# Kernel tuning notes

Measured on AMD Instinct MI355X. Metric: run time of the kernel, lower is better.

Reference implementation:

```python
import jax, jax.numpy as jnp
import numpy as np

# ---- static config (mirrors init_kwargs) ----
N, E, G = 10000, 120000, 32
F_NODE, F_EDGE = 64, 16
H, HEADS, L, R = 128, 4, 3, 4
ID_DIM, REL_DIM = 32, 8
NUM_IDS, NUM_CLASSES = 5000, 10
FFN_H, HEAD_H = 256, 128
GRID_SIZE, SPLINE_ORDER = 5, 3
NC = GRID_SIZE + SPLINE_ORDER  # n spline coeffs per input = 8
GRID = jnp.asarray(np.arange(-SPLINE_ORDER, GRID_SIZE + SPLINE_ORDER + 1, dtype=np.float32) * (2.0 / GRID_SIZE) - 1.0)  # [12], grid_range=(-1,1)
NEG = -1e30


def _b_splines(x, grid):
    # x: [B, in] -> bases [B, in, NC]  (Cox-de Boor, as in efficient-kan)
    x = x[..., None]
    bases = ((x >= grid[:-1]) & (x < grid[1:])).astype(x.dtype)
    for p in range(1, SPLINE_ORDER + 1):
        left = (x - grid[:-(p + 1)]) / (grid[p:-1] - grid[:-(p + 1)]) * bases[..., :-1]
        right = (grid[p + 1:] - x) / (grid[p + 1:] - grid[1:-p]) * bases[..., 1:]
        bases = left + right
    return bases


def _kan_linear(x, base_w, spline_w, scaler, grid):
    # base path: SiLU(x) @ W_base^T ; spline path: b_splines(x) contracted with scaled spline weights
    base = jax.nn.silu(x) @ base_w.T
    spline = jnp.einsum('big,oig->bo', _b_splines(x, grid), spline_w * scaler[..., None])
    return base + spline


def _ln(x, g, b, eps=1e-5):
    mu = x.mean(-1, keepdims=True)
    var = ((x - mu) ** 2).mean(-1, keepdims=True)
    return (x - mu) * jax.lax.rsqrt(var + eps) * g + b


def _forward(x, edge_attr, id_emb, in_W, in_b, Wl, bl, Wr, br, We, att, gat_bias,
             rel_gate, rel_emb, ln1_g, ln1_b, ln2_g, ln2_b,
             ffn1_base, ffn1_spline, ffn1_scaler, ffn2_base, ffn2_spline, ffn2_scaler,
             ro_g, ro_b, head1_base, head1_spline, head1_scaler, head2_base, head2_spline, head2_scaler,
             id_token, edge_index, edge_type, batch):
    grid = GRID
    # input proj: concat(id embedding) -> Linear -> SiLU (dropout = identity, eval)
    h = jnp.concatenate([x, id_emb[id_token]], axis=-1)
    h = jax.nn.silu(h @ in_W + in_b)
    src, tgt = edge_index[0], edge_index[1]
    for l in range(L):
        gates = jax.nn.softmax(rel_gate[l])  # all relations present
        h_msg = jnp.zeros_like(h)
        for r in range(R):
            # GATv2Conv (heads=4, concat=False, add_self_loops=False)
            xl = (h @ Wl[l, r] + bl[l, r]).reshape(N, HEADS, H)
            xr = (h @ Wr[l, r] + br[l, r]).reshape(N, HEADS, H)
            # edge feature = concat(edge_attr, rel_emb[r]) @ We, split to avoid materializing the concat
            e = (edge_attr @ We[l, r, :F_EDGE] + rel_emb[l, r] @ We[l, r, F_EDGE:]).reshape(E, HEADS, H)
            z = jax.nn.leaky_relu(xl[src] + xr[tgt] + e, 0.2)   # [E, heads, H]
            score = jnp.einsum('ehd,hd->eh', z, att[l, r])
            mask = (edge_type == r)[:, None]
            score = jnp.where(mask, score, NEG)
            m = jax.ops.segment_max(score, tgt, num_segments=N)  # per-target softmax max
            ex = jnp.where(mask, jnp.exp(score - m[tgt]), 0.0)
            denom = jax.ops.segment_sum(ex, tgt, num_segments=N)
            alpha = ex / jnp.maximum(denom[tgt], 1e-16)          # [E, heads]
            agg = jax.ops.segment_sum(xl[src] * alpha[..., None], tgt, num_segments=N)
            h_r = agg.mean(axis=1) + gat_bias[l, r]              # concat=False -> head mean + bias
            h_msg = h_msg + gates[r] * h_r
        h = _ln(h + h_msg, ln1_g[l], ln1_b[l])
        # KAN FFN: KANLinear(H->FFN_H) -> KANLinear(FFN_H->H)
        h_ffn = _kan_linear(h, ffn1_base[l], ffn1_spline[l], ffn1_scaler[l], grid)
        h_ffn = _kan_linear(h_ffn, ffn2_base[l], ffn2_spline[l], ffn2_scaler[l], grid)
        h = _ln(h + h_ffn, ln2_g[l], ln2_b[l])
    # readout: mean+max pool per graph
    cnt = jax.ops.segment_sum(jnp.ones((N,), h.dtype), batch, num_segments=G)
    h_mean = jax.ops.segment_sum(h, batch, num_segments=G) / jnp.maximum(cnt, 1.0)[:, None]
    h_max = jax.ops.segment_max(h, batch, num_segments=G)
    h_max = jnp.where(jnp.isfinite(h_max), h_max, 0.0)
    g = _ln(jnp.concatenate([h_mean, h_max], axis=-1), ro_g, ro_b)
    # KAN head: KANLinear(2H->HEAD_H) -> KANLinear(HEAD_H->NUM_CLASSES)
    g = _kan_linear(g, head1_base, head1_spline, head1_scaler, grid)
    logits = _kan_linear(g, head2_base, head2_spline, head2_scaler, grid)
    return logits


def setup_inputs():
    key = jax.random.key(0)
    ks = iter(jax.random.split(key, 48))
    n = lambda shape, s=0.05: jax.random.normal(next(ks), shape, dtype=jnp.float32) * s
    d = {}
    d['x'] = jax.random.normal(next(ks), (N, F_NODE), dtype=jnp.float32)
    d['edge_attr'] = jax.random.normal(next(ks), (E, F_EDGE), dtype=jnp.float32)
    d['id_token'] = jax.random.randint(next(ks), (N,), 0, NUM_IDS + 1)
    d['edge_index'] = jax.random.randint(next(ks), (2, E), 0, N)
    d['edge_type'] = jax.random.randint(next(ks), (E,), 0, R)
    d['batch'] = jnp.sort(jax.random.randint(next(ks), (N,), 0, G))
    d['id_emb'] = n((NUM_IDS + 1, ID_DIM), 0.1)
    d['in_W'] = n((F_NODE + ID_DIM, H))
    d['in_b'] = jnp.zeros((H,), jnp.float32)
    d['Wl'] = n((L, R, H, HEADS * H)); d['bl'] = jnp.zeros((L, R, HEADS * H), jnp.float32)
    d['Wr'] = n((L, R, H, HEADS * H)); d['br'] = jnp.zeros((L, R, HEADS * H), jnp.float32)
    d['We'] = n((L, R, F_EDGE + REL_DIM, HEADS * H))
    d['att'] = n((L, R, HEADS, H), 0.1)
    d['gat_bias'] = jnp.zeros((L, R, H), jnp.float32)
    d['rel_gate'] = n((L, R), 0.1)
    d['rel_emb'] = n((L, R, REL_DIM), 0.1)
    d['ln1_g'] = jnp.ones((L, H), jnp.float32); d['ln1_b'] = jnp.zeros((L, H), jnp.float32)
    d['ln2_g'] = jnp.ones((L, H), jnp.float32); d['ln2_b'] = jnp.zeros((L, H), jnp.float32)
    d['ffn1_base'] = n((L, FFN_H, H)); d['ffn1_spline'] = n((L, FFN_H, H, NC)); d['ffn1_scaler'] = jnp.ones((L, FFN_H, H), jnp.float32)
    d['ffn2_base'] = n((L, H, FFN_H)); d['ffn2_spline'] = n((L, H, FFN_H, NC)); d['ffn2_scaler'] = jnp.ones((L, H, FFN_H), jnp.float32)
    d['ro_g'] = jnp.ones((2 * H,), jnp.float32); d['ro_b'] = jnp.zeros((2 * H,), jnp.float32)
    d['head1_base'] = n((HEAD_H, 2 * H)); d['head1_spline'] = n((HEAD_H, 2 * H, NC)); d['head1_scaler'] = jnp.ones((HEAD_H, 2 * H), jnp.float32)
    d['head2_base'] = n((NUM_CLASSES, HEAD_H)); d['head2_spline'] = n((NUM_CLASSES, HEAD_H, NC)); d['head2_scaler'] = jnp.ones((NUM_CLASSES, HEAD_H), jnp.float32)
    return d


def reference(x, edge_attr, id_emb, in_W, in_b, Wl, bl, Wr, br, We, att, gat_bias,
              rel_gate, rel_emb, ln1_g, ln1_b, ln2_g, ln2_b,
              ffn1_base, ffn1_spline, ffn1_scaler, ffn2_base, ffn2_spline, ffn2_scaler,
              ro_g, ro_b, head1_base, head1_spline, head1_scaler, head2_base, head2_spline, head2_scaler,
              id_token, edge_index, edge_type, batch):
    return _forward(x, edge_attr, id_emb, in_W, in_b, Wl, bl, Wr, br, We, att, gat_bias,
                    rel_gate, rel_emb, ln1_g, ln1_b, ln2_g, ln2_b,
                    ffn1_base, ffn1_spline, ffn1_scaler, ffn2_base, ffn2_spline, ffn2_scaler,
                    ro_g, ro_b, head1_base, head1_spline, head1_scaler, head2_base, head2_spline, head2_scaler,
                    id_token, edge_index, edge_type, batch)
```

## Files before the change

### kernel.cpp

```cpp
#include <hip/hip_runtime.h>
#include <cstdint>
#include <cstddef>

#define NN      10000
#define NE      120000
#define NG      32
#define FNODE   64
#define FEDGE   16
#define HID     128
#define NHEADS  4
#define NL      3
#define NR      4
#define IDDIM   32
#define RELDIM  8
#define FFNH    256
#define HEADH   128
#define NCLS    10

#define NCHUNK  128
#define SCTOT   (NN * NR)
#define SCBLK   ((SCTOT + 255) / 256)

typedef __attribute__((ext_vector_type(8))) short short8;
typedef __attribute__((ext_vector_type(4))) float floatx4;

__device__ __forceinline__ float silu_f(float x) { return x / (1.f + expf(-x)); }
__device__ __forceinline__ ushort f2bf(float f) {
  unsigned u = __float_as_uint(f);
  return (ushort)((u + 0x7FFFu + ((u >> 16) & 1u)) >> 16);
}
__device__ __forceinline__ float bf2f(ushort h) { return __uint_as_float((unsigned)h << 16); }

__device__ __forceinline__ void kan_bases(float x, float* out8) {
  float bb[11];
#pragma unroll
  for (int j = 0; j < 11; ++j) {
    float t0 = (j - 3) * 0.4f - 1.f;
    float t1 = (j - 2) * 0.4f - 1.f;
    bb[j] = (x >= t0 && x < t1) ? 1.f : 0.f;
  }
  {
    const float inv = 1.f / 0.4f;
#pragma unroll
    for (int j = 0; j < 10; ++j) {
      float tj = (j - 3) * 0.4f - 1.f, tjp1 = (j - 1) * 0.4f - 1.f;
      bb[j] = ((x - tj) * bb[j] + (tjp1 - x) * bb[j + 1]) * inv;
    }
  }
  {
    const float inv = 1.f / 0.8f;
#pragma unroll
    for (int j = 0; j < 9; ++j) {
      float tj = (j - 3) * 0.4f - 1.f, tjp1 = (j) * 0.4f - 1.f;
      bb[j] = ((x - tj) * bb[j] + (tjp1 - x) * bb[j + 1]) * inv;
    }
  }
  {
    const float inv = 1.f / 1.2000001f;
#pragma unroll
    for (int j = 0; j < 8; ++j) {
      float tj = (j - 3) * 0.4f - 1.f, tjp1 = (j + 1) * 0.4f - 1.f;
      bb[j] = ((x - tj) * bb[j] + (tjp1 - x) * bb[j + 1]) * inv;
    }
  }
#pragma unroll
  for (int j = 0; j < 8; ++j) out8[j] = bb[j];
}

__global__ __launch_bounds__(256) void gemm_bf3(
    const ushort* __restrict__ Ahg, const ushort* __restrict__ Alg,
    const ushort* __restrict__ Bhg, const ushort* __restrict__ Blg,
    const float* __restrict__ bias, float* __restrict__ C,
    int M, int K, int N) {
  constexpr int LDA = 68;
  __shared__ __align__(16) ushort Ah[128 * LDA];
  __shared__ __align__(16) ushort Al[128 * LDA];
  __shared__ __align__(16) ushort Bh[64 * LDA];
  __shared__ __align__(16) ushort Bl[64 * LDA];
  const int tid = threadIdx.x;
  const int lane = tid & 63, wave = tid >> 6;
  const int lrow = lane & 15, quad = lane >> 4;
  const int bm = blockIdx.y * 128, bn = blockIdx.x * 64;
  floatx4 acc[2][4] = {};
  for (int k0 = 0; k0 < K; k0 += 64) {
#pragma unroll
    for (int i = 0; i < 4; ++i) {
      int c = tid + i * 256;
      int row = c >> 3, col8 = c & 7;
      int gr = bm + row;
      uint4 vh = make_uint4(0, 0, 0, 0), vl = make_uint4(0, 0, 0, 0);
      if (gr < M) {
        vh = *(const uint4*)(Ahg + (size_t)gr * K + k0 + col8 * 8);
        vl = *(const uint4*)(Alg + (size_t)gr * K + k0 + col8 * 8);
      }
      *(uint4*)&Ah[row * LDA + col8 * 8] = vh;
      *(uint4*)&Al[row * LDA + col8 * 8] = vl;
    }
#pragma unroll
    for (int i = 0; i < 2; ++i) {
      int c = tid + i * 256;
      int row = c >> 3, col8 = c & 7;
      *(uint4*)&Bh[row * LDA + col8 * 8] = *(const uint4*)(Bhg + (size_t)(bn + row) * K + k0 + col8 * 8);
      *(uint4*)&Bl[row * LDA + col8 * 8] = *(const uint4*)(Blg + (size_t)(bn + row) * K + k0 + col8 * 8);
    }
    __syncthreads();
#pragma unroll
    for (int kk = 0; kk < 64; kk += 32) {
      int kof = kk + quad * 8;
      const int ra0 = (wave * 32 + lrow) * LDA + kof;
      const int ra1 = (wave * 32 + 16 + lrow) * LDA + kof;
      short8 ah0 = *(const short8*)&Ah[ra0];
      short8 ah1 = *(const short8*)&Ah[ra1];
      short8 al0 = *(const short8*)&Al[ra0];
      short8 al1 = *(const short8*)&Al[ra1];
      short8 bh[4], blo[4];
#pragma unroll
      for (int nt = 0; nt < 4; ++nt) {
        int rb = (nt * 16 + lrow) * LDA + kof;
        bh[nt]  = *(const short8*)&Bh[rb];
        blo[nt] = *(const short8*)&Bl[rb];
      }
#pragma unroll
      for (int nt = 0; nt < 4; ++nt) {
        acc[0][nt] = __builtin_amdgcn_mfma_f32_16x16x32_bf16(ah0, bh[nt],  acc[0][nt], 0, 0, 0);
        acc[1][nt] = __builtin_amdgcn_mfma_f32_16x16x32_bf16(ah1, bh[nt],  acc[1][nt], 0, 0, 0);
        acc[0][nt] = __builtin_amdgcn_mfma_f32_16x16x32_bf16(al0, bh[nt],  acc[0][nt], 0, 0, 0);
        acc[1][nt] = __builtin_amdgcn_mfma_f32_16x16x32_bf16(al1, bh[nt],  acc[1][nt], 0, 0, 0);
        acc[0][nt] = __builtin_amdgcn_mfma_f32_16x16x32_bf16(ah0, blo[nt], acc[0][nt], 0, 0, 0);
        acc[1][nt] = __builtin_amdgcn_mfma_f32_16x16x32_bf16(ah1, blo[nt], acc[1][nt], 0, 0, 0);
      }
    }
    __syncthreads();
  }
#pragma unroll
  for (int mt = 0; mt < 2; ++mt) {
#pragma unroll
    for (int nt = 0; nt < 4; ++nt) {
#pragma unroll
      for (int reg = 0; reg < 4; ++reg) {
        int row = bm + wave * 32 + mt * 16 + quad * 4 + reg;
        int col = bn + nt * 16 + lrow;
        if (row < M) {
          float v = acc[mt][nt][reg];
          if (bias) v += bias[col];
          C[(size_t)row * N + col] = v;
        }
      }
    }
  }
}

template<int BM, int SPLIT>
__global__ __launch_bounds__(256) void gemm_kan(
    const float* __restrict__ A, const ushort* __restrict__ Bhg, const ushort* __restrict__ Blg,
    float* __restrict__ C, int M, int In, int N) {
  const int K = In * 9;
  const int ntiles = K >> 6;
  const int per = (ntiles + SPLIT - 1) / SPLIT;
  const int kt0 = blockIdx.z * per;
  const int kt1 = (kt0 + per < ntiles) ? (kt0 + per) : ntiles;
  constexpr int LDA = 68;
  __shared__ __align__(16) ushort Ah[BM * LDA];
  __shared__ __align__(16) ushort Al[BM * LDA];
  __shared__ __align__(16) ushort Bh[64 * LDA];
  __shared__ __align__(16) ushort Bl[64 * LDA];
  const int tid = threadIdx.x;
  const int lane = tid & 63, wave = tid >> 6;
  const int lrow = lane & 15, quad = lane >> 4;
  const int bm = blockIdx.y * BM, bn = blockIdx.x * 64;
  constexpr int MT = BM / 64;
  floatx4 acc[MT][4] = {};
  for (int kt = kt0; kt < kt1; ++kt) {
    int k0 = kt << 6;
    if (k0 < In) {
#pragma unroll
      for (int i = 0; i < BM / 16; ++i) {
        int c = tid + i * 256;
        int row = c >> 4, col4 = c & 15;
        int gr = bm + row;
        float4 v = make_float4(0.f, 0.f, 0.f, 0.f);
        if (gr < M) v = *(const float4*)(A + (size_t)gr * In + k0 + col4 * 4);
        float vv[4] = {silu_f(v.x), silu_f(v.y), silu_f(v.z), silu_f(v.w)};
        ushort h0 = f2bf(vv[0]), h1 = f2bf(vv[1]), h2 = f2bf(vv[2]), h3 = f2bf(vv[3]);
        ushort l0 = f2bf(vv[0] - bf2f(h0)), l1 = f2bf(vv[1] - bf2f(h1));
        ushort l2 = f2bf(vv[2] - bf2f(h2)), l3 = f2bf(vv[3] - bf2f(h3));
        *(uint2*)&Ah[row * LDA + col4 * 4] =
          make_uint2((unsigned)h0 | ((unsigned)h1 << 16), (unsigned)h2 | ((unsigned)h3 << 16));
        *(uint2*)&Al[row * LDA + col4 * 4] =
          make_uint2((unsigned)l0 | ((unsigned)l1 << 16), (unsigned)l2 | ((unsigned)l3 << 16));
      }
    } else {
      int i0 = (k0 - In) >> 3;
      if (tid < BM * 2) {
        int row = tid >> 1, half = tid & 1;
        int gr = bm + row;
        float4 v = make_float4(0.f, 0.f, 0.f, 0.f);
        if (gr < M) v = *(const float4*)(A + (size_t)gr * In + i0 + half * 4);
        float vv[4] = {v.x, v.y, v.z, v.w};
#pragma unroll
        for (int jj = 0; jj < 4; ++jj) {
          float b8[8];
          kan_bases(vv[jj], b8);
          unsigned hu[4], lu[4];
#pragma unroll
          for (int q = 0; q < 4; ++q) {
            ushort ha = f2bf(b8[2 * q]), hb = f2bf(b8[2 * q + 1]);
            ushort la = f2bf(b8[2 * q] - bf2f(ha)), lb = f2bf(b8[2 * q + 1] - bf2f(hb));
            hu[q] = (unsigned)ha | ((unsigned)hb << 16);
            lu[q] = (unsigned)la | ((unsigned)lb << 16);
          }
          int cbase = (half * 4 + jj) * 8;
          *(uint4*)&Ah[row * LDA + cbase] = make_uint4(hu[0], hu[1], hu[2], hu[3]);
          *(uint4*)&Al[row * LDA + cbase] = make_uint4(lu[0], lu[1], lu[2], lu[3]);
        }
      }
    }
#pragma unroll
    for (int i = 0; i < 2; ++i) {
      int c = tid + i * 256;
      int row = c >> 3, col8 = c & 7;
      *(uint4*)&Bh[row * LDA + col8 * 8] = *(const uint4*)(Bhg + (size_t)(bn + row) * K + k0 + col8 * 8);
      *(uint4*)&Bl[row * LDA + col8 * 8] = *(const uint4*)(Blg + (size_t)(bn + row) * K + k0 + col8 * 8);
    }
    __syncthreads();
#pragma unroll
    for (int kk = 0; kk < 64; kk += 32) {
      int kof = kk + quad * 8;
      short8 ah[MT], al[MT];
#pragma unroll
      for (int mt = 0; mt < MT; ++mt) {
        int ra = (wave * (BM / 4) + mt * 16 + lrow) * LDA + kof;
        ah[mt] = *(const short8*)&Ah[ra];
        al[mt] = *(const short8*)&Al[ra];
      }
      short8 bh[4], blo[4];
#pragma unroll
      for (int nt = 0; nt < 4; ++nt) {
        int rb = (nt * 16 + lrow) * LDA + kof;
        bh[nt]  = *(const short8*)&Bh[rb];
        blo[nt] = *(const short8*)&Bl[rb];
      }
#pragma unroll
      for (int nt = 0; nt < 4; ++nt) {
#pragma unroll
        for (int mt = 0; mt < MT; ++mt) {
          acc[mt][nt] = __builtin_amdgcn_mfma_f32_16x16x32_bf16(ah[mt], bh[nt],  acc[mt][nt], 0, 0, 0);
          acc[mt][nt] = __builtin_amdgcn_mfma_f32_16x16x32_bf16(al[mt], bh[nt],  acc[mt][nt], 0, 0, 0);
          acc[mt][nt] = __builtin_amdgcn_mfma_f32_16x16x32_bf16(ah[mt], blo[nt], acc[mt][nt], 0, 0, 0);
        }
      }
    }
    __syncthreads();
  }
#pragma unroll
  for (int mt = 0; mt < MT; ++mt) {
#pragma unroll
    for (int nt = 0; nt < 4; ++nt) {
#pragma unroll
      for (int reg = 0; reg < 4; ++reg) {
        int row = bm + wave * (BM / 4) + mt * 16 + quad * 4 + reg;
        int col = bn + nt * 16 + lrow;
        if (row < M) atomicAdd(&C[(size_t)row * N + col], acc[mt][nt][reg]);
      }
    }
  }
}

__global__ void conv_wT2(const float* __restrict__ Wl, const float* __restrict__ Wr,
                         const float* __restrict__ bl, const float* __restrict__ br,
                         ushort* __restrict__ WTh, ushort* __restrict__ WTl,
                         float* __restrict__ bout, int total) {
  int i = blockIdx.x * 256 + threadIdx.x;
  if (i >= total) return;
  int g2 = i / (2048 * 128), rem = i % (2048 * 128);
  int n = rem >> 7, k = rem & 127;
  int l = g2 >> 1, pair = g2 & 1;
  int r = pair * 2 + (n >> 10);
  int nsub = n & 1023;
  int nn = nsub & 511;
  int g = l * NR + r;
  const float* W = (nsub < 512) ? Wl : Wr;
  float v = W[(size_t)g * 65536 + (size_t)k * 512 + nn];
  ushort hi = f2bf(v);
  WTh[i] = hi;
  WTl[i] = f2bf(v - bf2f(hi));
  if (k == 0) bout[g2 * 2048 + n] = ((nsub < 512) ? bl : br)[g * 512 + nn];
}

__global__ void build_kan_wT(const float* __restrict__ base_w, const float* __restrict__ spline_w,
                             const float* __restrict__ scaler,
                             ushort* __restrict__ BTh, ushort* __restrict__ BTl,
                             int In, int Out) {
  int i = blockIdx.x * 256 + threadIdx.x;
  if (i >= In * 9 * Out) return;
  int o = i / (In * 9), k = i % (In * 9);
  float v;
  if (k < In) v = base_w[(size_t)o * In + k];
  else {
    int q = k - In, ii = q >> 3, gq = q & 7;
    v = spline_w[((size_t)o * In + ii) * 8 + gq] * scaler[(size_t)o * In + ii];
  }
  ushort hi = f2bf(v);
  BTh[i] = hi;
  BTl[i] = f2bf(v - bf2f(hi));
}

__global__ __launch_bounds__(128) void input_proj(
    const float* __restrict__ x, const float* __restrict__ id_emb,
    const int* __restrict__ id_token, const float* __restrict__ inW,
    const float* __restrict__ inb, float* __restrict__ h,
    ushort* __restrict__ hh, ushort* __restrict__ hl) {
  int n = blockIdx.x, j = threadIdx.x;
  __shared__ float s[FNODE + IDDIM];
  if (j < FNODE) s[j] = x[(size_t)n * FNODE + j];
  else if (j < FNODE + IDDIM) s[j] = id_emb[(size_t)id_token[n] * IDDIM + (j - FNODE)];
  __syncthreads();
  float acc = inb[j];
#pragma unroll
  for (int k = 0; k < FNODE + IDDIM; ++k) acc = fmaf(s[k], inW[k * HID + j], acc);
  float v = silu_f(acc);
  h[(size_t)n * HID + j] = v;
  ushort hi = f2bf(v);
  hh[(size_t)n * HID + j] = hi;
  hl[(size_t)n * HID + j] = f2bf(v - bf2f(hi));
}

__global__ __launch_bounds__(512) void layer_prep(
    const float* __restrict__ rel_gate, const float* __restrict__ gat_bias,
    const float* __restrict__ rel_emb, const float* __restrict__ We, int l,
    float* __restrict__ gates, float* __restrict__ msg_bias, float* __restrict__ erel) {
  int j = threadIdx.x;
  float g[NR]; float mx = -1e30f;
  for (int r = 0; r < NR; ++r) { g[r] = rel_gate[l * NR + r]; mx = fmaxf(mx, g[r]); }
  float s = 0.f;
  for (int r = 0; r < NR; ++r) { g[r] = expf(g[r] - mx); s += g[r]; }
  for (int r = 0; r < NR; ++r) g[r] /= s;
  if (j < NR) gates[j] = g[j];
  if (j < HID) {
    float b = 0.f;
    for (int r = 0; r < NR; ++r) b = fmaf(g[r], gat_bias[((size_t)(l * NR + r)) * HID + j], b);
    msg_bias[j] = b;
  }
  for (int r = 0; r < NR; ++r) {
    const float* Wer = We + ((size_t)(l * NR + r)) * 24 * 512;
    const float* re  = rel_emb + (l * NR + r) * RELDIM;
    float acc = 0.f;
#pragma unroll
    for (int q = 0; q < RELDIM; ++q) acc = fmaf(re[q], Wer[(FEDGE + q) * 512 + j], acc);
    erel[r * 512 + j] = acc;
  }
}

__global__ void fill_zero(float* __restrict__ p, int n) {
  int i = blockIdx.x * 256 + threadIdx.x;
  if (i < n) p[i] = 0.f;
}
__global__ void fill_zero_i(int* __restrict__ p, int n) {
  int i = blockIdx.x * 256 + threadIdx.x;
  if (i < n) p[i] = 0;
}

__global__ void csr_count2(const int* __restrict__ eidx, const int* __restrict__ etype,
                           int* __restrict__ deg2) {
  int e = blockIdx.x * 256 + threadIdx.x;
  if (e < NE) atomicAdd(&deg2[eidx[NE + e] * NR + etype[e]], 1);
}

__global__ __launch_bounds__(256) void scan_p1(const int* __restrict__ deg2,
                                               int* __restrict__ tmp_incl, int* __restrict__ bsum) {
  __shared__ int ps[256];
  int t = threadIdx.x, blk = blockIdx.x;
  int i = blk * 256 + t;
  int v = (i < SCTOT) ? deg2[i] : 0;
  ps[t] = v;
  __syncthreads();
  for (int o = 1; o < 256; o <<= 1) {
    int u = (t >= o) ? ps[t - o] : 0;
    __syncthreads();
    ps[t] += u;
    __syncthreads();
  }
  if (i < SCTOT) tmp_incl[i] = ps[t];
  if (t == 255) bsum[blk] = ps[255];
}
__global__ __launch_bounds__(256) void scan_p2(const int* __restrict__ bsum, int* __restrict__ boff) {
  __shared__ int ps[256];
  int t = threadIdx.x;
  int v = (t < SCBLK) ? bsum[t] : 0;
  ps[t] = v;
  __syncthreads();
  for (int o = 1; o < 256; o <<= 1) {
    int u = (t >= o) ? ps[t - o] : 0;
    __syncthreads();
    ps[t] += u;
    __syncthreads();
  }
  if (t < SCBLK) boff[t] = ps[t] - v;
}
__global__ __launch_bounds__(256) void scan_p3(const int* __restrict__ deg2,
                                               const int* __restrict__ tmp_incl,
                                               const int* __restrict__ boff,
                                               int* __restrict__ in_off2, int* __restrict__ cursor2) {
  int t = threadIdx.x, blk = blockIdx.x;
  int i = blk * 256 + t;
  if (i < SCTOT) {
    int excl = boff[blk] + tmp_incl[i] - deg2[i];
    in_off2[i] = excl;
    cursor2[i] = excl;
  }
  if (i == 0) in_off2[SCTOT] = NE;
}

__global__ void csr_scatter2(const int* __restrict__ eidx, const int* __restrict__ etype,
                             int* __restrict__ cursor2,
                             int* __restrict__ in_e2, int* __restrict__ in_s2) {
  int e = blockIdx.x * 256 + threadIdx.x;
  if (e < NE) {
    int pos = atomicAdd(&cursor2[eidx[NE + e] * NR + etype[e]], 1);
    in_e2[pos] = e;
    in_s2[pos] = eidx[e];
  }
}

__global__ __launch_bounds__(256) void gat_node6(
    const int* __restrict__ in_off2, const int* __restrict__ in_e2, const int* __restrict__ in_s2,
    const float* __restrict__ eattr, const float* __restrict__ xlr,
    const float* __restrict__ We_base, const float* __restrict__ erel_base,
    const float* __restrict__ att_base, const float* __restrict__ gates,
    int rbase, float* __restrict__ hmsg) {
  __shared__ __align__(16) float WeL[16 * 512];
  __shared__ __align__(16) float sAgg[4][512];
  int tid = threadIdx.x;
  int rs = blockIdx.y;
  int r = rbase + rs;
  const float* We_r = We_base + (size_t)rs * 24 * 512;
  for (int i = tid; i < 16 * 512 / 4; i += 256)
    *(float4*)&WeL[i * 4] = *(const float4*)&We_r[i * 4];
  __syncthreads();
  float gr = gates[r] * 0.25f;
  int lane = tid & 63, wave = tid >> 6;
  int n = blockIdx.x * 4 + wave;
  if (n >= NN) return;
  int roff = rs * 1024;
  const int cA = lane * 4;
  const int cB = 256 + lane * 4;
  const float* xrb = xlr + (size_t)n * 2048 + roff + 512;
  float4 xrA = *(const float4*)(xrb + cA);
  float4 xrB = *(const float4*)(xrb + cB);
  float4 attA = *(const float4*)(att_base + rs * 512 + cA);
  float4 attB = *(const float4*)(att_base + rs * 512 + cB);
  float4 erA  = *(const float4*)(erel_base + rs * 512 + cA);
  float4 erB  = *(const float4*)(erel_base + rs * 512 + cB);
  float mA = -1e30f, mB = -1e30f, lsA = 0.f, lsB = 0.f;
  float4 accA = make_float4(0.f, 0.f, 0.f, 0.f);
  float4 accB = make_float4(0.f, 0.f, 0.f, 0.f);
  int e0 = in_off2[n * NR + r];
  int cnt = in_off2[n * NR + r + 1] - e0;
  float4 pxA, pxB, pe0, pe1, pe2, pe3;
  int eN = 0, sN = 0;
  if (cnt > 0) {
    int eC = in_e2[e0], sC = in_s2[e0];
    if (cnt > 1) { eN = in_e2[e0 + 1]; sN = in_s2[e0 + 1]; }
    const float* xls = xlr + (size_t)sC * 2048 + roff;
    pxA = *(const float4*)(xls + cA);
    pxB = *(const float4*)(xls + cB);
    const float4* eap = (const float4*)(eattr + (size_t)eC * 16);
    pe0 = eap[0]; pe1 = eap[1]; pe2 = eap[2]; pe3 = eap[3];
  }
  for (int j = 0; j < cnt; ++j) {
    float4 xA = pxA, xB = pxB;
    float ea[16] = {pe0.x, pe0.y, pe0.z, pe0.w, pe1.x, pe1.y, pe1.z, pe1.w,
                    pe2.x, pe2.y, pe2.z, pe2.w, pe3.x, pe3.y, pe3.z, pe3.w};
    if (j + 1 < cnt) {
      int eC = eN, sC = sN;
      if (j + 2 < cnt) { eN = in_e2[e0 + j + 2]; sN = in_s2[e0 + j + 2]; }
      const float* xls = xlr + (size_t)sC * 2048 + roff;
      pxA = *(const float4*)(xls + cA);
      pxB = *(const float4*)(xls + cB);
      const float4* eap = (const float4*)(eattr + (size_t)eC * 16);
      pe0 = eap[0]; pe1 = eap[1]; pe2 = eap[2]; pe3 = eap[3];
    }
    float4 etA = erA, etB = erB;
#pragma unroll
    for (int k = 0; k < 16; ++k) {
      float4 wA = *(const float4*)&WeL[k * 512 + cA];
      float4 wB = *(const float4*)&WeL[k * 512 + cB];
      etA.x = fmaf(ea[k], wA.x, etA.x); etA.y = fmaf(ea[k], wA.y, etA.y);
      etA.z = fmaf(ea[k], wA.z, etA.z); etA.w = fmaf(ea[k], wA.w, etA.w);
      etB.x = fmaf(ea[k], wB.x, etB.x); etB.y = fmaf(ea[k], wB.y, etB.y);
      etB.z = fmaf(ea[k], wB.z, etB.z); etB.w = fmaf(ea[k], wB.w, etB.w);
    }
    float sA, sB;
    {
      float z0 = xA.x + xrA.x + etA.x; z0 = (z0 > 0.f) ? z0 : 0.2f * z0;
      float z1 = xA.y + xrA.y + etA.y; z1 = (z1 > 0.f) ? z1 : 0.2f * z1;
      float z2 = xA.z + xrA.z + etA.z; z2 = (z2 > 0.f) ? z2 : 0.2f * z2;
      float z3 = xA.w + xrA.w + etA.w; z3 = (z3 > 0.f) ? z3 : 0.2f * z3;
      sA = z0 * attA.x + z1 * attA.y + z2 * attA.z + z3 * attA.w;
      z0 = xB.x + xrB.x + etB.x; z0 = (z0 > 0.f) ? z0 : 0.2f * z0;
      z1 = xB.y + xrB.y + etB.y; z1 = (z1 > 0.f) ? z1 : 0.2f * z1;
      z2 = xB.z + xrB.z + etB.z; z2 = (z2 > 0.f) ? z2 : 0.2f * z2;
      z3 = xB.w + xrB.w + etB.w; z3 = (z3 > 0.f) ? z3 : 0.2f * z3;
      sB = z0 * attB.x + z1 * attB.y + z2 * attB.z + z3 * attB.w;
    }
#pragma unroll
    for (int o = 1; o <= 16; o <<= 1) {
      sA += __shfl_xor(sA, o, 64);
      sB += __shfl_xor(sB, o, 64);
    }
    {
      float mn = fmaxf(mA, sA);
      float sc = expf(mA - mn), we = expf(sA - mn);
      mA = mn; lsA = lsA * sc + we;
      accA.x = accA.x * sc + we * xA.x; accA.y = accA.y * sc + we * xA.y;
      accA.z = accA.z * sc + we * xA.z; accA.w = accA.w * sc + we * xA.w;
    }
    {
      float mn = fmaxf(mB, sB);
      float sc = expf(mB - mn), we = expf(sB - mn);
      mB = mn; lsB = lsB * sc + we;
      accB.x = accB.x * sc + we * xB.x; accB.y = accB.y * sc + we * xB.y;
      accB.z = accB.z * sc + we * xB.z; accB.w = accB.w * sc + we * xB.w;
    }
  }
  float invA = 1.f / fmaxf(lsA, 1e-16f);
  float invB = 1.f / fmaxf(lsB, 1e-16f);
  *(float4*)&sAgg[wave][cA] = make_float4(accA.x * invA, accA.y * invA, accA.z * invA, accA.w * invA);
  *(float4*)&sAgg[wave][cB] = make_float4(accB.x * invB, accB.y * invB, accB.z * invB, accB.w * invB);
  float o0 = sAgg[wave][lane]       + sAgg[wave][128 + lane]
           + sAgg[wave][256 + lane] + sAgg[wave][384 + lane];
  float o1 = sAgg[wave][64 + lane]  + sAgg[wave][192 + lane]
           + sAgg[wave][320 + lane] + sAgg[wave][448 + lane];
  size_t base = (size_t)n * HID;
  atomicAdd(&hmsg[base + lane],      gr * o0);
  atomicAdd(&hmsg[base + 64 + lane], gr * o1);
}

__global__ __launch_bounds__(64) void ln128(
    float* __restrict__ h, const float* __restrict__ add, const float* __restrict__ bvec,
    const float* __restrict__ g, const float* __restrict__ b,
    ushort* __restrict__ hh, ushort* __restrict__ hl) {
  int n = blockIdx.x, lane = threadIdx.x;
  size_t base = (size_t)n * HID;
  float x0 = h[base + lane] + add[base + lane];
  float x1 = h[base + 64 + lane] + add[base + 64 + lane];
  if (bvec) { x0 += bvec[lane]; x1 += bvec[64 + lane]; }
  float s = x0 + x1;
#pragma unroll
  for (int m = 32; m > 0; m >>= 1) s += __shfl_xor(s, m, 64);
  float mu = s * (1.f / 128.f);
  float d0 = x0 - mu, d1 = x1 - mu;
  float q = d0 * d0 + d1 * d1;
#pragma unroll
  for (int m = 32; m > 0; m >>= 1) q += __shfl_xor(q, m, 64);
  float inv = 1.f / sqrtf(q * (1.f / 128.f) + 1e-5f);
  float o0 = d0 * inv * g[lane] + b[lane];
  float o1 = d1 * inv * g[64 + lane] + b[64 + lane];
  h[base + lane]      = o0;
  h[base + 64 + lane] = o1;
  if (hh) {
    ushort i0 = f2bf(o0), i1 = f2bf(o1);
    hh[base + lane] = i0;        hh[base + 64 + lane] = i1;
    hl[base + lane] = f2bf(o0 - bf2f(i0));
    hl[base + 64 + lane] = f2bf(o1 - bf2f(i1));
  }
}

__global__ void expand_f32(const float* __restrict__ v, float* __restrict__ u, int In, int rows) {
  int i = blockIdx.x * 256 + threadIdx.x;
  if (i >= rows * In) return;
  int n = i / In, c = i % In;
  float x = v[(size_t)n * In + c];
  size_t base = (size_t)n * In * 9;
  u[base + c] = silu_f(x);
  float b8[8];
  kan_bases(x, b8);
  float* ub = u + base + In + (size_t)c * 8;
#pragma unroll
  for (int gq = 0; gq < 8; ++gq) ub[gq] = b8[gq];
}

__global__ __launch_bounds__(128) void pool_part(
    const float* __restrict__ h, const int* __restrict__ batch,
    float* __restrict__ psum, float* __restrict__ pmax, float* __restrict__ pcnt) {
  __shared__ float sS[NG][HID];
  __shared__ float sM[NG][HID];
  __shared__ int sC[NG];
  int d = threadIdx.x, blk = blockIdx.x;
  const float NEGINF = __uint_as_float(0xff800000u);
  for (int i = d; i < NG * HID; i += 128) {
    ((float*)sS)[i] = 0.f;
    ((float*)sM)[i] = NEGINF;
  }
  if (d < NG) sC[d] = 0;
  __syncthreads();
  const int CH = (NN + NCHUNK - 1) / NCHUNK;
  int n0 = blk * CH, n1 = (n0 + CH < NN) ? n0 + CH : NN;
  for (int n = n0; n < n1; ++n) {
    int g = batch[n];
    float v = h[(size_t)n * HID + d];
    sS[g][d] += v;
    sM[g][d] = fmaxf(sM[g][d], v);
    if (d == 0) sC[g]++;
  }
  __syncthreads();
  for (int i = d; i < NG * HID; i += 128) {
    psum[(size_t)blk * NG * HID + i] = ((float*)sS)[i];
    pmax[(size_t)blk * NG * HID + i] = ((float*)sM)[i];
  }
  if (d < NG) pcnt[blk * NG + d] = (float)sC[d];
}

__global__ __launch_bounds__(256) void pool_final2(
    const float* __restrict__ psum, const float* __restrict__ pmax,
    const float* __restrict__ pcnt, const float* __restrict__ rog,
    const float* __restrict__ rob, float* __restrict__ gvec) {
  int g = blockIdx.x, j = threadIdx.x;
  __shared__ float rb[256];
  float x;
  if (j < HID) {
    float s = 0.f, cn = 0.f;
    for (int c = 0; c < NCHUNK; ++c) {
      s += psum[(size_t)c * NG * HID + g * HID + j];
      cn += pcnt[c * NG + g];
    }
    x = s / fmaxf(cn, 1.f);
  } else {
    float mx = __uint_as_float(0xff800000u);
    for (int c = 0; c < NCHUNK; ++c)
      mx = fmaxf(mx, pmax[(size_t)c * NG * HID + g * HID + (j - HID)]);
    x = (mx > -1e38f) ? mx : 0.f;
  }
  rb[j] = x; __syncthreads();
  for (int st = 128; st > 0; st >>= 1) { if (j < st) rb[j] += rb[j + st]; __syncthreads(); }
  float mu = rb[0] * (1.f / 256.f); __syncthreads();
  float d = x - mu;
  rb[j] = d * d; __syncthreads();
  for (int st = 128; st > 0; st >>= 1) { if (j < st) rb[j] += rb[j + st]; __syncthreads(); }
  float var = rb[0] * (1.f / 256.f);
  float inv = 1.f / sqrtf(var + 1e-5f);
  gvec[(size_t)g * 256 + j] = d * inv * rog[j] + rob[j];
}

__global__ __launch_bounds__(256) void kan_head_w(
    const float* __restrict__ u, const float* __restrict__ base_w,
    const float* __restrict__ spline_w, const float* __restrict__ scaler,
    float* __restrict__ out, int In, int Out, int npairs) {
  int wid = blockIdx.x * 4 + (threadIdx.x >> 6);
  if (wid >= npairs) return;
  int g = wid / Out, o = wid % Out;
  int lane = threadIdx.x & 63;
  const float* ug = u + (size_t)g * In * 9;
  const float* bw = base_w + (size_t)o * In;
  const float* sp = spline_w + (size_t)o * In * 8;
  const float* sc = scaler + (size_t)o * In;
  float acc = 0.f;
  for (int i = lane; i < In; i += 64) acc = fmaf(ug[i], bw[i], acc);
  const float* us = ug + In;
  for (int k = lane; k < In * 8; k += 64) {
    int i = k >> 3;
    acc = fmaf(us[k], sp[k] * sc[i], acc);
  }
#pragma unroll
  for (int off2 = 32; off2 > 0; off2 >>= 1) acc += __shfl_xor(acc, off2, 64);
  if (lane == 0) out[(size_t)g * Out + o] = acc;
}

extern "C" void kernel_launch(void* const* d_in, const int* in_sizes, int n_in,
                              void* d_out, int out_size, void* d_ws, size_t ws_size,
                              hipStream_t stream) {
  const float* x         = (const float*)d_in[0];
  const float* edge_attr = (const float*)d_in[1];
  const int*   id_token  = (const int*)  d_in[2];
  const int*   edge_index= (const int*)  d_in[3];
  const int*   edge_type = (const int*)  d_in[4];
  const int*   batch     = (const int*)  d_in[5];
  const float* id_emb    = (const float*)d_in[6];
  const float* inW       = (const float*)d_in[7];
  const float* inb       = (const float*)d_in[8];
  const float* Wl        = (const float*)d_in[9];
  const float* bl        = (const float*)d_in[10];
  const float* Wr        = (const float*)d_in[11];
  const float* br        = (const float*)d_in[12];
  const float* We        = (const float*)d_in[13];
  const float* att       = (const float*)d_in[14];
  const float* gat_bias  = (const float*)d_in[15];
  const float* rel_gate  = (const float*)d_in[16];
  const float* rel_emb   = (const float*)d_in[17];
  const float* ln1g      = (const float*)d_in[18];
  const float* ln1b      = (const float*)d_in[19];
  const float* ln2g      = (const float*)d_in[20];
  const float* ln2b      = (const float*)d_in[21];
  const float* ffn1_base = (const float*)d_in[22];
  const float* ffn1_spl  = (const float*)d_in[23];
  const float* ffn1_sc   = (const float*)d_in[24];
  const float* ffn2_base = (const float*)d_in[25];
  const float* ffn2_spl  = (const float*)d_in[26];
  const float* ffn2_sc   = (const float*)d_in[27];
  const float* rog       = (const float*)d_in[28];
  const float* rob       = (const float*)d_in[29];
  const float* h1_base   = (const float*)d_in[30];
  const float* h1_spl    = (const float*)d_in[31];
  const float* h1_sc     = (const float*)d_in[32];
  const float* h2_base   = (const float*)d_in[33];
  const float* h2_spl    = (const float*)d_in[34];
  const float* h2_sc     = (const float*)d_in[35];
  (void)in_sizes; (void)n_in; (void)out_size; (void)ws_size;

  char* wsp = (char*)d_ws;
  size_t off = 0;
  auto carve = [&](size_t bytes) { char* p = wsp + off; off = (off + bytes + 255) & ~(size_t)255; return p; };
  float*    h     = (float*)   carve((size_t)NN * HID * 4);
  ushort*   h_hi  = (ushort*)  carve((size_t)NN * HID * 2);
  ushort*   h_lo  = (ushort*)  carve((size_t)NN * HID * 2);
  float*    hmsg  = (float*)   carve((size_t)NN * HID * 4);
  float*    t1    = (float*)   carve((size_t)NN * FFNH * 4);
  float*    gates = (float*)   carve(NR * 4);
  float*    msgb  = (float*)   carve(HID * 4);
  float*    erel  = (float*)   carve(NR * 512 * 4);
  ushort*   WTh   = (ushort*)  carve((size_t)NL * 2 * 2048 * HID * 2);
  ushort*   WTl   = (ushort*)  carve((size_t)NL * 2 * 2048 * HID * 2);
  float*    blr   = (float*)   carve((size_t)NL * 2 * 2048 * 4);
  ushort*   B1h   = (ushort*)  carve((size_t)FFNH * HID * 9 * 2);
  ushort*   B1l   = (ushort*)  carve((size_t)FFNH * HID * 9 * 2);
  ushort*   B2h   = (ushort*)  carve((size_t)HID * FFNH * 9 * 2);
  ushort*   B2l   = (ushort*)  carve((size_t)HID * FFNH * 9 * 2);
  float*    psum  = (float*)   carve((size_t)NCHUNK * NG * HID * 4);
  float*    pmax  = (float*)   carve((size_t)NCHUNK * NG * HID * 4);
  float*    pcnt  = (float*)   carve((size_t)NCHUNK * NG * 4);
  float*    gvec  = (float*)   carve((size_t)NG * 256 * 4);
  float*    uhead = (float*)   carve((size_t)NG * 256 * 9 * 4);
  float*    thead = (float*)   carve((size_t)NG * HEADH * 4);
  float*    xlr   = (float*)   carve((size_t)NN * 2048 * 4);
  int*      deg2  = (int*)     carve((size_t)SCTOT * 4);
  int*      in_off2=(int*)     carve((size_t)(SCTOT + 1) * 4);
  int*      cursor2=(int*)     carve((size_t)SCTOT * 4);
  int*      tmp_incl=(int*)    carve((size_t)SCTOT * 4);
  int*      bsum  = (int*)     carve((size_t)SCBLK * 4);
  int*      boff  = (int*)     carve((size_t)SCBLK * 4);
  int*      in_e2 = (int*)     carve((size_t)NE * 4);
  int*      in_s2 = (int*)     carve((size_t)NE * 4);

  fill_zero_i<<<(SCTOT + 255) / 256, 256, 0, stream>>>(deg2, SCTOT);
  csr_count2<<<(NE + 255) / 256, 256, 0, stream>>>(edge_index, edge_type, deg2);
  scan_p1<<<SCBLK, 256, 0, stream>>>(deg2, tmp_incl, bsum);
  scan_p2<<<1, 256, 0, stream>>>(bsum, boff);
  scan_p3<<<SCBLK, 256, 0, stream>>>(deg2, tmp_incl, boff, in_off2, cursor2);
  csr_scatter2<<<(NE + 255) / 256, 256, 0, stream>>>(edge_index, edge_type, cursor2, in_e2, in_s2);

  {
    int total = NL * 2 * 2048 * 128;
    conv_wT2<<<(total + 255) / 256, 256, 0, stream>>>(Wl, Wr, bl, br, WTh, WTl, blr, total);
  }

  input_proj<<<NN, 128, 0, stream>>>(x, id_emb, id_token, inW, inb, h, h_hi, h_lo);

  const int MB128 = (NN + 127) / 128;
  const int MB64  = (NN + 63) / 64;
  for (int l = 0; l < NL; ++l) {
    layer_prep<<<1, 512, 0, stream>>>(rel_gate, gat_bias, rel_emb, We, l, gates, msgb, erel);
    fill_zero<<<(NN * HID + 255) / 256, 256, 0, stream>>>(hmsg, NN * HID);
    for (int pair = 0; pair < 2; ++pair) {
      int g2 = l * 2 + pair;
      const ushort* WThp = WTh + (size_t)g2 * 2048 * HID;
      const ushort* WTlp = WTl + (size_t)g2 * 2048 * HID;
      const float* blp   = blr + (size_t)g2 * 2048;
      int rbase = pair * 2;
      gemm_bf3<<<dim3(2048 / 64, MB128), 256, 0, stream>>>(h_hi, h_lo, WThp, WTlp, blp, xlr, NN, HID, 2048);
      gat_node6<<<dim3((NN + 3) / 4, 2), 256, 0, stream>>>(
          in_off2, in_e2, in_s2, edge_attr, xlr,
          We + ((size_t)(l * NR + rbase)) * 24 * 512, erel + rbase * 512,
          att + (size_t)(l * NR + rbase) * 512, gates, rbase, hmsg);
    }
    ln128<<<NN, 64, 0, stream>>>(h, hmsg, msgb, ln1g + l * HID, ln1b + l * HID, nullptr, nullptr);

    build_kan_wT<<<((HID * 9 * FFNH) + 255) / 256, 256, 0, stream>>>(
        ffn1_base + (size_t)l * FFNH * HID, ffn1_spl + (size_t)l * FFNH * HID * 8,
        ffn1_sc + (size_t)l * FFNH * HID, B1h, B1l, HID, FFNH);
    fill_zero<<<(NN * FFNH + 255) / 256, 256, 0, stream>>>(t1, NN * FFNH);
    gemm_kan<128, 3><<<dim3(FFNH / 64, MB128, 3), 256, 0, stream>>>(h, B1h, B1l, t1, NN, HID, FFNH);
    build_kan_wT<<<((FFNH * 9 * HID) + 255) / 256, 256, 0, stream>>>(
        ffn2_base + (size_t)l * HID * FFNH, ffn2_spl + (size_t)l * HID * FFNH * 8,
        ffn2_sc + (size_t)l * HID * FFNH, B2h, B2l, FFNH, HID);
    fill_zero<<<(NN * HID + 255) / 256, 256, 0, stream>>>(hmsg, NN * HID);
    gemm_kan<64, 4><<<dim3(HID / 64, MB64, 4), 256, 0, stream>>>(t1, B2h, B2l, hmsg, NN, FFNH, HID);
    ln128<<<NN, 64, 0, stream>>>(h, hmsg, nullptr, ln2g + l * HID, ln2b + l * HID, h_hi, h_lo);
  }

  pool_part<<<NCHUNK, 128, 0, stream>>>(h, batch, psum, pmax, pcnt);
  pool_final2<<<NG, 256, 0, stream>>>(psum, pmax, pcnt, rog, rob, gvec);
  expand_f32<<<((NG * 256) + 255) / 256, 256, 0, stream>>>(gvec, uhead, 256, NG);
  {
    int npairs = NG * HEADH;
    kan_head_w<<<(npairs + 3) / 4, 256, 0, stream>>>(uhead, h1_base, h1_spl, h1_sc, thead, 256, HEADH, npairs);
  }
  expand_f32<<<((NG * HEADH) + 255) / 256, 256, 0, stream>>>(thead, uhead, HEADH, NG);
  {
    int npairs = NG * NCLS;
    kan_head_w<<<(npairs + 3) / 4, 256, 0, stream>>>(uhead, h2_base, h2_spl, h2_sc, (float*)d_out, HEADH, NCLS, npairs);
  }
}
```

Measured before the change: 1.492 ms.

## Retile KAN GEMM to 64-row by wide-N tiles, spreading spline basis work

The KAN GEMM tile changes from BM rows by 64 columns to 64 rows by NT*16 columns, with each wave computing one 16-row strip across NT column tiles. The spline-basis computation is now spread over all 256 threads (two inputs each) instead of a subset doing four, which cuts per-thread serial basis work and keeps every thread busy. Wider N tiles mean each basis tile is computed fewer times across the grid, cutting redundant Cox-de Boor evaluation. The cost is more B-tile loads per block and a different grid shape and occupancy.

```diff
diff --git a/kernel.cpp b/kernel.cpp
--- a/kernel.cpp
+++ b/kernel.cpp
@@ -150,7 +150,7 @@
   }
 }
 
-template<int BM, int SPLIT>
+template<int NT, int SPLIT>
 __global__ __launch_bounds__(256) void gemm_kan(
     const float* __restrict__ A, const ushort* __restrict__ Bhg, const ushort* __restrict__ Blg,
     float* __restrict__ C, int M, int In, int N) {
@@ -160,21 +160,21 @@
   const int kt0 = blockIdx.z * per;
   const int kt1 = (kt0 + per < ntiles) ? (kt0 + per) : ntiles;
   constexpr int LDA = 68;
-  __shared__ __align__(16) ushort Ah[BM * LDA];
-  __shared__ __align__(16) ushort Al[BM * LDA];
-  __shared__ __align__(16) ushort Bh[64 * LDA];
-  __shared__ __align__(16) ushort Bl[64 * LDA];
+  constexpr int BN = NT * 16;
+  __shared__ __align__(16) ushort Ah[64 * LDA];
+  __shared__ __align__(16) ushort Al[64 * LDA];
+  __shared__ __align__(16) ushort Bh[BN * LDA];
+  __shared__ __align__(16) ushort Bl[BN * LDA];
   const int tid = threadIdx.x;
   const int lane = tid & 63, wave = tid >> 6;
   const int lrow = lane & 15, quad = lane >> 4;
-  const int bm = blockIdx.y * BM, bn = blockIdx.x * 64;
-  constexpr int MT = BM / 64;
-  floatx4 acc[MT][4] = {};
+  const int bm = blockIdx.y * 64, bn = blockIdx.x * BN;
+  floatx4 acc[NT] = {};
   for (int kt = kt0; kt < kt1; ++kt) {
     int k0 = kt << 6;
     if (k0 < In) {
 #pragma unroll
-      for (int i = 0; i < BM / 16; ++i) {
+      for (int i = 0; i < 4; ++i) {
         int c = tid + i * 256;
         int row = c >> 4, col4 = c & 15;
         int gr = bm + row;
@@ -191,32 +191,30 @@
       }
     } else {
       int i0 = (k0 - In) >> 3;
-      if (tid < BM * 2) {
-        int row = tid >> 1, half = tid & 1;
-        int gr = bm + row;
-        float4 v = make_float4(0.f, 0.f, 0.f, 0.f);
-        if (gr < M) v = *(const float4*)(A + (size_t)gr * In + i0 + half * 4);
-        float vv[4] = {v.x, v.y, v.z, v.w};
-#pragma unroll
-        for (int jj = 0; jj < 4; ++jj) {
-          float b8[8];
-          kan_bases(vv[jj], b8);
-          unsigned hu[4], lu[4];
-#pragma unroll
-          for (int q = 0; q < 4; ++q) {
-            ushort ha = f2bf(b8[2 * q]), hb = f2bf(b8[2 * q + 1]);
-            ushort la = f2bf(b8[2 * q] - bf2f(ha)), lb = f2bf(b8[2 * q + 1] - bf2f(hb));
-            hu[q] = (unsigned)ha | ((unsigned)hb << 16);
-            lu[q] = (unsigned)la | ((unsigned)lb << 16);
-          }
-          int cbase = (half * 4 + jj) * 8;
-          *(uint4*)&Ah[row * LDA + cbase] = make_uint4(hu[0], hu[1], hu[2], hu[3]);
-          *(uint4*)&Al[row * LDA + cbase] = make_uint4(lu[0], lu[1], lu[2], lu[3]);
+      int row = tid >> 2, q = tid & 3;
+      int gr = bm + row;
+      float2 v = make_float2(0.f, 0.f);
+      if (gr < M) v = *(const float2*)(A + (size_t)gr * In + i0 + q * 2);
+      float vv[2] = {v.x, v.y};
+#pragma unroll
+      for (int jj = 0; jj < 2; ++jj) {
+        float b8[8];
+        kan_bases(vv[jj], b8);
+        unsigned hu[4], lu[4];
+#pragma unroll
+        for (int p = 0; p < 4; ++p) {
+          ushort ha = f2bf(b8[2 * p]), hb = f2bf(b8[2 * p + 1]);
+          ushort la = f2bf(b8[2 * p] - bf2f(ha)), lb = f2bf(b8[2 * p + 1] - bf2f(hb));
+          hu[p] = (unsigned)ha | ((unsigned)hb << 16);
+          lu[p] = (unsigned)la | ((unsigned)lb << 16);
         }
+        int cbase = (q * 2 + jj) * 8;
+        *(uint4*)&Ah[row * LDA + cbase] = make_uint4(hu[0], hu[1], hu[2], hu[3]);
+        *(uint4*)&Al[row * LDA + cbase] = make_uint4(lu[0], lu[1], lu[2], lu[3]);
       }
     }
 #pragma unroll
-    for (int i = 0; i < 2; ++i) {
+    for (int i = 0; i < NT / 2; ++i) {
       int c = tid + i * 256;
       int row = c >> 3, col8 = c & 7;
       *(uint4*)&Bh[row * LDA + col8 * 8] = *(const uint4*)(Bhg + (size_t)(bn + row) * K + k0 + col8 * 8);
@@ -226,42 +224,28 @@
 #pragma unroll
     for (int kk = 0; kk < 64; kk += 32) {
       int kof = kk + quad * 8;
-      short8 ah[MT], al[MT];
-#pragma unroll
-      for (int mt = 0; mt < MT; ++mt) {
-        int ra = (wave * (BM / 4) + mt * 16 + lrow) * LDA + kof;
-        ah[mt] = *(const short8*)&Ah[ra];
-        al[mt] = *(const short8*)&Al[ra];
+      int ra = (wave * 16 + lrow) * LDA + kof;
+      short8 ah = *(const short8*)&Ah[ra];
+      short8 al = *(const short8*)&Al[ra];
+#pragma unroll
+      for (int nt = 0; nt < NT; ++nt) {
+        int rb = (nt * 16 + lrow) * LDA + kof;
+        short8 bh  = *(const short8*)&Bh[rb];
+        short8 blo = *(const short8*)&Bl[rb];
+        acc[nt] = __builtin_amdgcn_mfma_f32_16x16x32_bf16(ah, bh,  acc[nt], 0, 0, 0);
+        acc[nt] = __builtin_amdgcn_mfma_f32_16x16x32_bf16(al, bh,  acc[nt], 0, 0, 0);
+        acc[nt] = __builtin_amdgcn_mfma_f32_16x16x32_bf16(ah, blo, acc[nt], 0, 0, 0);
       }
-      short8 bh[4], blo[4];
-#pragma unroll
-      for (int nt = 0; nt < 4; ++nt) {
-        int rb = (nt * 16 + lrow) * LDA + kof;
-        bh[nt]  = *(const short8*)&Bh[rb];
-        blo[nt] = *(const short8*)&Bl[rb];
-      }
-#pragma unroll
-      for (int nt = 0; nt < 4; ++nt) {
-#pragma unroll
-        for (int mt = 0; mt < MT; ++mt) {
-          acc[mt][nt] = __builtin_amdgcn_mfma_f32_16x16x32_bf16(ah[mt], bh[nt],  acc[mt][nt], 0, 0, 0);
-          acc[mt][nt] = __builtin_amdgcn_mfma_f32_16x16x32_bf16(al[mt], bh[nt],  acc[mt][nt], 0, 0, 0);
-          acc[mt][nt] = __builtin_amdgcn_mfma_f32_16x16x32_bf16(ah[mt], blo[nt], acc[mt][nt], 0, 0, 0);
-        }
-      }
     }
     __syncthreads();
   }
 #pragma unroll
-  for (int mt = 0; mt < MT; ++mt) {
-#pragma unroll
-    for (int nt = 0; nt < 4; ++nt) {
-#pragma unroll
-      for (int reg = 0; reg < 4; ++reg) {
-        int row = bm + wave * (BM / 4) + mt * 16 + quad * 4 + reg;
-        int col = bn + nt * 16 + lrow;
-        if (row < M) atomicAdd(&C[(size_t)row * N + col], acc[mt][nt][reg]);
-      }
+  for (int nt = 0; nt < NT; ++nt) {
+#pragma unroll
+    for (int reg = 0; reg < 4; ++reg) {
+      int row = bm + wave * 16 + quad * 4 + reg;
+      int col = bn + nt * 16 + lrow;
+      if (row < M) atomicAdd(&C[(size_t)row * N + col], acc[nt][reg]);
     }
   }
 }
@@ -778,12 +762,12 @@
         ffn1_base + (size_t)l * FFNH * HID, ffn1_spl + (size_t)l * FFNH * HID * 8,
         ffn1_sc + (size_t)l * FFNH * HID, B1h, B1l, HID, FFNH);
     fill_zero<<<(NN * FFNH + 255) / 256, 256, 0, stream>>>(t1, NN * FFNH);
-    gemm_kan<128, 3><<<dim3(FFNH / 64, MB128, 3), 256, 0, stream>>>(h, B1h, B1l, t1, NN, HID, FFNH);
+    gemm_kan<8, 3><<<dim3(FFNH / 128, MB64, 3), 256, 0, stream>>>(h, B1h, B1l, t1, NN, HID, FFNH);
     build_kan_wT<<<((FFNH * 9 * HID) + 255) / 256, 256, 0, stream>>>(
         ffn2_base + (size_t)l * HID * FFNH, ffn2_spl + (size_t)l * HID * FFNH * 8,
         ffn2_sc + (size_t)l * HID * FFNH, B2h, B2l, FFNH, HID);
     fill_zero<<<(NN * HID + 255) / 256, 256, 0, stream>>>(hmsg, NN * HID);
-    gemm_kan<64, 4><<<dim3(HID / 64, MB64, 4), 256, 0, stream>>>(t1, B2h, B2l, hmsg, NN, FFNH, HID);
+    gemm_kan<8, 4><<<dim3(HID / 128, MB64, 4), 256, 0, stream>>>(t1, B2h, B2l, hmsg, NN, FFNH, HID);
     ln128<<<NN, 64, 0, stream>>>(h, hmsg, nullptr, ln2g + l * HID, ln2b + l * HID, h_hi, h_lo);
   }
 
```

Result: no change. 1.473 ms (-1.3%).
